# Kernel optimization log

Hardware: AMD Instinct MI355X
Metric: run time of the kernel (lower is better)

The kernel has to match this reference:

```python
import jax, jax.numpy as jnp
import numpy as np

N = 100000
E = 600000
G = 8
HID = 128
HEADS = 4
C = HID // HEADS  # 32


def setup_inputs() -> dict:
    key = jax.random.key(0)
    ks = jax.random.split(key, 32)
    s = 0.05
    node_numeric = jax.random.normal(ks[0], (N, 8), jnp.float32)
    node_cat0 = jax.random.randint(ks[1], (N,), 0, 32)
    node_cat1 = jax.random.randint(ks[2], (N,), 0, 64)
    edge_numeric = jax.random.normal(ks[3], (E, 4), jnp.float32)
    edge_cat0 = jax.random.randint(ks[4], (E,), 0, 16)
    edge_cat1 = jax.random.randint(ks[5], (E,), 0, 100)
    src = jax.random.randint(ks[6], (E,), 0, N)
    dst = jax.random.randint(ks[7], (E,), 0, N)
    dst = jnp.where(dst == src, (dst + 1) % N, dst)  # GATConv removes self-loops before adding its own
    edge_index = jnp.stack([src, dst])
    batch = jnp.sort(jax.random.randint(ks[8], (N,), 0, G))
    recipe = jax.random.normal(ks[9], (G, 16), jnp.float32)
    return dict(
        node_numeric=node_numeric, node_cat0=node_cat0, node_cat1=node_cat1,
        edge_numeric=edge_numeric, edge_cat0=edge_cat0, edge_cat1=edge_cat1,
        edge_index=edge_index, batch=batch, recipe=recipe,
        emb_node0=jax.random.normal(ks[10], (32, 6), jnp.float32) * s,
        emb_node1=jax.random.normal(ks[11], (64, 8), jnp.float32) * s,
        emb_edge0=jax.random.normal(ks[12], (16, 4), jnp.float32) * s,
        emb_edge1=jax.random.normal(ks[13], (100, 10), jnp.float32) * s,
        W_in=jax.random.normal(ks[14], (38, HID), jnp.float32) * s,
        b_in=jnp.zeros((HID,), jnp.float32),
        W_edge=jax.random.normal(ks[15], (18, HID), jnp.float32) * s,
        b_edge=jnp.zeros((HID,), jnp.float32),
        gat_lin=jax.random.normal(ks[16], (3, HID, HID), jnp.float32) * s,
        gat_lin_edge=jax.random.normal(ks[17], (3, HID, HID), jnp.float32) * s,
        att_src=jax.random.normal(ks[18], (3, HEADS, C), jnp.float32) * s,
        att_dst=jax.random.normal(ks[19], (3, HEADS, C), jnp.float32) * s,
        att_edge=jax.random.normal(ks[20], (3, HEADS, C), jnp.float32) * s,
        gat_bias=jnp.zeros((3, HID), jnp.float32),
        W_r1=jax.random.normal(ks[21], (HID, HID), jnp.float32) * s,
        b_r1=jnp.zeros((HID,), jnp.float32),
        W_r2=jax.random.normal(ks[22], (HID, 1), jnp.float32) * s,
        b_r2=jnp.zeros((1,), jnp.float32),
    )


def _segment_softmax(logits, seg, num):
    m = jax.ops.segment_max(logits, seg, num_segments=num)
    ex = jnp.exp(logits - m[seg])
    s = jax.ops.segment_sum(ex, seg, num_segments=num)
    return ex / s[seg]


def _forward(node_numeric, edge_numeric, recipe,
             emb_node0, emb_node1, emb_edge0, emb_edge1,
             W_in, b_in, W_edge, b_edge,
             gat_lin, gat_lin_edge, att_src, att_dst, att_edge, gat_bias,
             W_r1, b_r1, W_r2, b_r2,
             node_cat0, node_cat1, edge_cat0, edge_cat1, edge_index, batch):
    n = node_numeric.shape[0]
    src, dst = edge_index[0], edge_index[1]
    # node encoding: numeric + categorical embeddings + broadcast recipe
    h = jnp.concatenate([node_numeric, emb_node0[node_cat0], emb_node1[node_cat1], recipe[batch]], axis=1)
    h = jax.nn.relu(h @ W_in + b_in)
    # edge encoding (shared across GAT layers)
    e = jnp.concatenate([edge_numeric, emb_edge0[edge_cat0], emb_edge1[edge_cat1]], axis=1)
    e = e @ W_edge + b_edge
    # self-loops with fill_value='mean': per-dst mean of incoming edge_attr
    cnt = jax.ops.segment_sum(jnp.ones((e.shape[0],), e.dtype), dst, num_segments=n)
    loop = jax.ops.segment_sum(e, dst, num_segments=n) / jnp.maximum(cnt, 1.0)[:, None]
    ar = jnp.arange(n)
    src_a = jnp.concatenate([src, ar])
    dst_a = jnp.concatenate([dst, ar])
    e_a = jnp.concatenate([e, loop], axis=0)  # [E+N, HID]
    for l in range(gat_lin.shape[0]):
        x = (h @ gat_lin[l]).reshape(n, HEADS, C)          # shared lin_src/lin_dst
        ee = (e_a @ gat_lin_edge[l]).reshape(-1, HEADS, C)
        a_s = jnp.sum(x * att_src[l], axis=-1)   # [N, HEADS]
        a_d = jnp.sum(x * att_dst[l], axis=-1)
        a_e = jnp.sum(ee * att_edge[l], axis=-1)  # [E+N, HEADS]
        logits = jax.nn.leaky_relu(a_s[src_a] + a_d[dst_a] + a_e, negative_slope=0.2)
        alpha = _segment_softmax(logits, dst_a, n)  # segment softmax over dst
        out = jax.ops.segment_sum(x[src_a] * alpha[:, :, None], dst_a, num_segments=n)
        h = jax.nn.relu(out.reshape(n, HID) + gat_bias[l])  # dropout off (eval)
    g = jax.ops.segment_sum(h, batch, num_segments=G)  # global_add_pool
    g = jax.nn.relu(g @ W_r1 + b_r1)
    return g @ W_r2 + b_r2  # [G, 1]


def reference(node_numeric, node_cat0, node_cat1, edge_numeric, edge_cat0, edge_cat1,
              edge_index, batch, recipe,
              emb_node0, emb_node1, emb_edge0, emb_edge1,
              W_in, b_in, W_edge, b_edge,
              gat_lin, gat_lin_edge, att_src, att_dst, att_edge, gat_bias,
              W_r1, b_r1, W_r2, b_r2):
    return _forward(node_numeric, edge_numeric, recipe,
                    emb_node0, emb_node1, emb_edge0, emb_edge1,
                    W_in, b_in, W_edge, b_edge,
                    gat_lin, gat_lin_edge, att_src, att_dst, att_edge, gat_bias,
                    W_r1, b_r1, W_r2, b_r2,
                    node_cat0, node_cat1, edge_cat0, edge_cat1, edge_index, batch)
```

## Files before the change

kernel.cpp:

```cpp
#include <hip/hip_runtime.h>
#include <math.h>

#define HID 128

typedef float f32x4 __attribute__((ext_vector_type(4)));
typedef short bf16x8 __attribute__((ext_vector_type(8)));
typedef unsigned int uint32;

__device__ __forceinline__ float leaky02(float z) { return z >= 0.f ? z : 0.2f * z; }
__device__ __forceinline__ unsigned short f2bf(float f) {
  uint32 u = __float_as_uint(f);
  u = (u + 0x7fff + ((u >> 16) & 1)) >> 16;
  return (unsigned short)u;
}
__device__ __forceinline__ float bf2f(uint32 us) { return __uint_as_float(us << 16); }
__device__ __forceinline__ float bflo(uint32 w) { return __uint_as_float(w << 16); }
__device__ __forceinline__ float bfhi(uint32 w) { return __uint_as_float(w & 0xffff0000u); }

__global__ void k_enc(const float* __restrict__ nodenum, const int* __restrict__ c0,
                      const int* __restrict__ c1, const int* __restrict__ batch,
                      const float* __restrict__ recipe,
                      const float* __restrict__ e0, const float* __restrict__ e1,
                      const float* __restrict__ Win, const float* __restrict__ bin,
                      unsigned short* __restrict__ hb, int n) {
  __shared__ float f[8][40];
  __shared__ int idx[8][3];
  int t = threadIdx.x;
  int col = t & 127;
  int half = t >> 7;
  float w[40];
#pragma unroll
  for (int k = 0; k < 38; k++) w[k] = Win[k * 128 + col];
  w[38] = 0.f;
  w[39] = 0.f;
  float bias = bin[col];
  int ntiles = (n + 7) / 8;
  for (int tile = blockIdx.x; tile < ntiles; tile += gridDim.x) {
    int base = tile * 8;
    if (t < 64) {
      int r = t >> 3, k = t & 7;
      int v = base + r;
      f[r][k] = (v < n) ? nodenum[(size_t)v * 8 + k] : 0.f;
    } else if (t < 88) {
      int j = t - 64;
      int r = j / 3, which = j - r * 3;
      int v = base + r;
      int val = 0;
      if (v < n) val = (which == 0) ? c0[v] : ((which == 1) ? c1[v] : batch[v]);
      idx[r][which] = val;
    } else if (t >= 240) {
      int r = t - 240;
      if (r < 8) { f[r][38] = 0.f; f[r][39] = 0.f; }
    }
    __syncthreads();
    if (t < 240) {
      int r = t / 30, k = t - r * 30;
      float val;
      if (k < 6) val = e0[idx[r][0] * 6 + k];
      else if (k < 14) val = e1[idx[r][1] * 8 + (k - 6)];
      else val = recipe[idx[r][2] * 16 + (k - 14)];
      f[r][8 + k] = val;
    }
    __syncthreads();
#pragma unroll
    for (int rr = 0; rr < 4; rr++) {
      int r = half * 4 + rr;
      int v = base + r;
      float acc = bias;
#pragma unroll
      for (int k4 = 0; k4 < 10; k4++) {
        float4 fv = *(const float4*)(&f[r][k4 * 4]);
        acc += fv.x * w[k4 * 4] + fv.y * w[k4 * 4 + 1] + fv.z * w[k4 * 4 + 2] +
               fv.w * w[k4 * 4 + 3];
      }
      if (v < n) hb[(size_t)v * 128 + col] = f2bf(fmaxf(acc, 0.f));
    }
    __syncthreads();
  }
}

__global__ void k_prep(const float* __restrict__ gle, const float* __restrict__ atte,
                       const float* __restrict__ We, const float* __restrict__ be,
                       float* __restrict__ P, float* __restrict__ q) {
  __shared__ float M[128 * 4];
  int t = threadIdx.x;
  for (int l = 0; l < 3; l++) {
    {
      int k = t;
#pragma unroll
      for (int hh = 0; hh < 4; hh++) {
        float acc = 0.f;
        for (int c = 0; c < 32; c++)
          acc += gle[l * 16384 + k * 128 + hh * 32 + c] * atte[l * 128 + hh * 32 + c];
        M[k * 4 + hh] = acc;
      }
    }
    __syncthreads();
    if (t < 72) {
      int j = t >> 2, hh = t & 3;
      float acc = 0.f;
      for (int k = 0; k < 128; k++) acc += We[j * 128 + k] * M[k * 4 + hh];
      P[(l * 18 + j) * 4 + hh] = acc;
    }
    if (t < 4) {
      float acc = 0.f;
      for (int k = 0; k < 128; k++) acc += be[k] * M[k * 4 + t];
      q[l * 4 + t] = acc;
    }
    __syncthreads();
  }
}

__global__ void k_wprep(const float* __restrict__ glin, unsigned short* __restrict__ WbfT) {
  int idx = blockIdx.x * 256 + threadIdx.x;
  if (idx >= 3 * 128 * 128) return;
  int l = idx >> 14;
  int rem = idx & 16383;
  int col = rem >> 7;
  int k = rem & 127;
  WbfT[idx] = f2bf(glin[(l << 14) + k * 128 + col]);
}

__global__ void k_deg(const int* __restrict__ dst, int* __restrict__ cnt, int E) {
  int i = blockIdx.x * 256 + threadIdx.x;
  if (i < E) atomicAdd(&cnt[dst[i]], 1);
}

__global__ void k_ae(const float* __restrict__ enum_, const int* __restrict__ ec0,
                     const int* __restrict__ ec1, const int* __restrict__ dst,
                     const int* __restrict__ srcarr,
                     const float* __restrict__ ee0, const float* __restrict__ ee1,
                     const float* __restrict__ P, const float* __restrict__ q,
                     int* __restrict__ cursor, float* __restrict__ ae3,
                     int* __restrict__ srcc, int E) {
  __shared__ float Ps[216];
  __shared__ float qs[12];
  int t = threadIdx.x;
  for (int i = t; i < 216; i += 256) Ps[i] = P[i];
  if (t < 12) qs[t] = q[t];
  __syncthreads();
  int i = blockIdx.x * 256 + t;
  if (i >= E) return;
  float raw[18];
  float4 nm = *(const float4*)(enum_ + (size_t)i * 4);
  raw[0] = nm.x; raw[1] = nm.y; raw[2] = nm.z; raw[3] = nm.w;
  int a0 = ec0[i], a1 = ec1[i];
  float4 eb0 = *(const float4*)(ee0 + a0 * 4);
  raw[4] = eb0.x; raw[5] = eb0.y; raw[6] = eb0.z; raw[7] = eb0.w;
#pragma unroll
  for (int j = 0; j < 10; j++) raw[8 + j] = ee1[a1 * 10 + j];
  int d = dst[i];
  int pos = atomicAdd(&cursor[d], 1);
  srcc[pos] = srcarr[i];
#pragma unroll
  for (int l = 0; l < 3; l++) {
    float o[4];
#pragma unroll
    for (int hh = 0; hh < 4; hh++) {
      float acc = qs[l * 4 + hh];
#pragma unroll
      for (int j = 0; j < 18; j++) acc += raw[j] * Ps[(l * 18 + j) * 4 + hh];
      o[hh] = acc;
    }
    *(float4*)(ae3 + ((size_t)l * E + pos) * 4) = make_float4(o[0], o[1], o[2], o[3]);
  }
}

__global__ void k_loopmean(const float* __restrict__ ae3, const int* __restrict__ rowptr,
                           float* __restrict__ aeL, int n, int E) {
  int v = blockIdx.x * 256 + threadIdx.x;
  if (v >= n) return;
  int beg = rowptr[v], end = rowptr[v + 1];
  float inv = (end > beg) ? 1.f / (float)(end - beg) : 0.f;
#pragma unroll
  for (int l = 0; l < 3; l++) {
    float4 s = make_float4(0.f, 0.f, 0.f, 0.f);
    const float4* base = (const float4*)(ae3 + (size_t)l * E * 4);
    for (int j = beg; j < end; j++) {
      float4 a = base[j];
      s.x += a.x; s.y += a.y; s.z += a.z; s.w += a.w;
    }
    *(float4*)(aeL + ((size_t)l * n + v) * 4) =
        make_float4(s.x * inv, s.y * inv, s.z * inv, s.w * inv);
  }
}

__global__ void k_scan1(const int* __restrict__ cnt, int* __restrict__ excl,
                        int* __restrict__ bsum, int n) {
  __shared__ int sh[256];
  int t = threadIdx.x;
  int i = blockIdx.x * 256 + t;
  int v = (i < n) ? cnt[i] : 0;
  sh[t] = v;
  __syncthreads();
  for (int off = 1; off < 256; off <<= 1) {
    int add = (t >= off) ? sh[t - off] : 0;
    __syncthreads();
    sh[t] += add;
    __syncthreads();
  }
  if (i < n) excl[i] = sh[t] - v;
  if (t == 255) bsum[blockIdx.x] = sh[255];
}

__global__ void k_scan2(int* __restrict__ bsum, int nb) {
  __shared__ int sh[512];
  int t = threadIdx.x;
  int v = (t < nb) ? bsum[t] : 0;
  sh[t] = v;
  __syncthreads();
  for (int off = 1; off < 512; off <<= 1) {
    int add = (t >= off) ? sh[t - off] : 0;
    __syncthreads();
    sh[t] += add;
    __syncthreads();
  }
  if (t < nb) bsum[t] = sh[t] - v;
}

__global__ void k_scan3(int* __restrict__ rowptr, const int* __restrict__ boff,
                        int* __restrict__ cursor, int n, int E) {
  int i = blockIdx.x * 256 + threadIdx.x;
  if (i < n) {
    int val = rowptr[i] + boff[i >> 8];
    rowptr[i] = val;
    cursor[i] = val;
  }
  if (i == 0) rowptr[n] = E;
}

__global__ void __launch_bounds__(512, 4)
k_x(const unsigned short* __restrict__ hb, const unsigned short* __restrict__ WbfT,
    const float* __restrict__ att_s, const float* __restrict__ att_d,
    unsigned short* __restrict__ xb, float* __restrict__ a_s,
    float* __restrict__ a_d, int n) {
  __shared__ unsigned short hs[64 * 128];
  int t = threadIdx.x;
  int w = t >> 6, l = t & 63;
  int ch = w >> 2, wr = w & 3;
  int lr = l & 15, lg = l >> 4;
  bf16x8 bfrag[4][4];
#pragma unroll
  for (int ct = 0; ct < 4; ct++) {
#pragma unroll
    for (int ks = 0; ks < 4; ks++) {
      int col = ch * 64 + ct * 16 + lr;
      int k0 = ks * 32 + lg * 8;
      bfrag[ct][ks] = *(const bf16x8*)(WbfT + col * 128 + k0);
    }
  }
  float avs[4], avd[4];
#pragma unroll
  for (int ct = 0; ct < 4; ct++) {
    avs[ct] = att_s[ch * 64 + ct * 16 + lr];
    avd[ct] = att_d[ch * 64 + ct * 16 + lr];
  }
  for (int tb = blockIdx.x * 64; tb < n; tb += gridDim.x * 64) {
    __syncthreads();
#pragma unroll
    for (int i = 0; i < 2; i++) {
      int idx = t + i * 512;
      int r = idx >> 4, c = idx & 15;
      uint4 vv = make_uint4(0, 0, 0, 0);
      if (tb + r < n) vv = *(const uint4*)(hb + (size_t)(tb + r) * 128 + c * 8);
      *(uint4*)(&hs[r * 128 + ((c ^ (r & 7)) * 8)]) = vv;
    }
    __syncthreads();
    f32x4 acc[4];
#pragma unroll
    for (int ct = 0; ct < 4; ct++) acc[ct] = (f32x4){0.f, 0.f, 0.f, 0.f};
#pragma unroll
    for (int ks = 0; ks < 4; ks++) {
      int r = wr * 16 + lr;
      int c = ks * 4 + lg;
      bf16x8 a = *(const bf16x8*)(&hs[r * 128 + ((c ^ (r & 7)) * 8)]);
#pragma unroll
      for (int ct = 0; ct < 4; ct++)
        acc[ct] = __builtin_amdgcn_mfma_f32_16x16x32_bf16(a, bfrag[ct][ks], acc[ct], 0, 0, 0);
    }
#pragma unroll
    for (int j = 0; j < 4; j++) {
      int row = tb + wr * 16 + lg * 4 + j;
      bool ok = row < n;
      if (ok) {
#pragma unroll
        for (int ct = 0; ct < 4; ct++)
          xb[(size_t)row * 128 + ch * 64 + ct * 16 + lr] = f2bf(acc[ct][j]);
      }
      float psA = acc[0][j] * avs[0] + acc[1][j] * avs[1];
      float pdA = acc[0][j] * avd[0] + acc[1][j] * avd[1];
      float psB = acc[2][j] * avs[2] + acc[3][j] * avs[3];
      float pdB = acc[2][j] * avd[2] + acc[3][j] * avd[3];
#pragma unroll
      for (int m = 1; m <= 8; m <<= 1) {
        psA += __shfl_xor(psA, m); pdA += __shfl_xor(pdA, m);
        psB += __shfl_xor(psB, m); pdB += __shfl_xor(pdB, m);
      }
      if (lr == 0 && ok) {
        a_s[(size_t)row * 4 + ch * 2] = psA;
        a_s[(size_t)row * 4 + ch * 2 + 1] = psB;
        a_d[(size_t)row * 4 + ch * 2] = pdA;
        a_d[(size_t)row * 4 + ch * 2 + 1] = pdB;
      }
    }
  }
}

__global__ void k_agg(const unsigned short* __restrict__ xb, const float* __restrict__ a_s,
                      const float* __restrict__ a_d, const float* __restrict__ ae3,
                      const float* __restrict__ aeL,
                      const int* __restrict__ rowptr, const int* __restrict__ srcc,
                      const float* __restrict__ bias,
                      unsigned short* __restrict__ hbout, int n, int E, int l) {
  int wid = threadIdx.x >> 6;
  int v = blockIdx.x * 4 + wid;
  if (v >= n) return;
  int lane = threadIdx.x & 63;
  int el = lane >> 2;
  int hh = lane & 3;
  float ad_own = a_d[(size_t)v * 4 + hh];
  float as_own = a_s[(size_t)v * 4 + hh];
  float aeL_own = aeL[((size_t)l * n + v) * 4 + hh];
  float m_own = leaky02(as_own + ad_own + aeL_own);
  float s_own = 1.f;
  int c2 = lane * 2;
  int headO = lane >> 4;
  const char* xB = (const char*)xb;
  uint32 coff = (uint32)c2 * 2u;
  uint32 wv = *(const uint32*)(xB + ((uint32)v << 8) + coff);
  float a0 = bflo(wv);
  float a1 = bfhi(wv);
  int beg = rowptr[v], end = rowptr[v + 1];
  const float* aeB = ae3 + (size_t)l * E * 4;
  for (int cb = beg; cb < end; cb += 16) {
    int ne = end - cb;
    if (ne > 16) ne = 16;
    float logit = -1e30f;
    int srcE = 0;
    if (el < ne) {
      int j = cb + el;
      srcE = srcc[j];
      float asrc = a_s[(size_t)srcE * 4 + hh];
      float aev = aeB[(size_t)j * 4 + hh];
      logit = leaky02(asrc + ad_own + aev);
    }
    float cm = logit;
    cm = fmaxf(cm, __shfl_xor(cm, 4));
    cm = fmaxf(cm, __shfl_xor(cm, 8));
    cm = fmaxf(cm, __shfl_xor(cm, 16));
    cm = fmaxf(cm, __shfl_xor(cm, 32));
    float mn_own = fmaxf(m_own, cm);
    float p = (el < ne) ? __expf(logit - mn_own) : 0.f;
    float ps = p;
    ps += __shfl_xor(ps, 4);
    ps += __shfl_xor(ps, 8);
    ps += __shfl_xor(ps, 16);
    ps += __shfl_xor(ps, 32);
    float c_own = __expf(m_own - mn_own);
    m_own = mn_own;
    s_own = s_own * c_own + ps;
    float cO = __shfl(c_own, headO);
    a0 *= cO;
    a1 *= cO;
    int e = 0;
    for (; e + 2 <= ne; e += 2) {
      int se0 = __builtin_amdgcn_readlane(srcE, e * 4);
      int se1 = __builtin_amdgcn_readlane(srcE, e * 4 + 4);
      float p0 = __shfl(p, e * 4 + headO);
      float p1 = __shfl(p, e * 4 + 4 + headO);
      uint32 x0 = *(const uint32*)(xB + ((uint32)se0 << 8) + coff);
      uint32 x1 = *(const uint32*)(xB + ((uint32)se1 << 8) + coff);
      a0 += p0 * bflo(x0) + p1 * bflo(x1);
      a1 += p0 * bfhi(x0) + p1 * bfhi(x1);
    }
    if (e < ne) {
      int se = __builtin_amdgcn_readlane(srcE, e * 4);
      float pC = __shfl(p, e * 4 + headO);
      uint32 xw = *(const uint32*)(xB + ((uint32)se << 8) + coff);
      a0 += pC * bflo(xw);
      a1 += pC * bfhi(xw);
    }
  }
  float sO = __shfl(s_own, headO);
  float r0 = fmaxf(a0 / sO + bias[l * HID + c2], 0.f);
  float r1 = fmaxf(a1 / sO + bias[l * HID + c2 + 1], 0.f);
  uint32 pk = (uint32)f2bf(r0) | ((uint32)f2bf(r1) << 16);
  *(uint32*)(hbout + (size_t)v * HID + c2) = pk;
}

__global__ void k_pool(const unsigned short* __restrict__ hb, const int* __restrict__ batch,
                       float* __restrict__ g, int n) {
  int t = threadIdx.x;
  int per = (n + gridDim.x - 1) / gridDim.x;
  int start = blockIdx.x * per;
  int end = min(n, start + per);
  float acc = 0.f;
  int cur = -1;
  for (int v = start; v < end; v++) {
    int b = batch[v];
    if (b != cur) {
      if (cur >= 0) atomicAdd(&g[cur * 128 + t], acc);
      acc = 0.f;
      cur = b;
    }
    acc += bf2f((uint32)hb[(size_t)v * 128 + t]);
  }
  if (cur >= 0) atomicAdd(&g[cur * 128 + t], acc);
}

__global__ void k_head(const float* __restrict__ g, const float* __restrict__ Wr1,
                       const float* __restrict__ br1, const float* __restrict__ Wr2,
                       const float* __restrict__ br2, float* __restrict__ out, int G_) {
  __shared__ float gl[8 * 128];
  __shared__ float red[128];
  int t = threadIdx.x;
  for (int i = t; i < G_ * 128; i += 128) gl[i] = g[i];
  __syncthreads();
  for (int i = 0; i < G_; i++) {
    float acc = br1[t];
    for (int k = 0; k < 128; k++) acc += gl[i * 128 + k] * Wr1[k * 128 + t];
    float hv = fmaxf(acc, 0.f);
    red[t] = hv * Wr2[t];
    __syncthreads();
    if (t == 0) {
      float s = br2[0];
      for (int k = 0; k < 128; k++) s += red[k];
      out[i] = s;
    }
    __syncthreads();
  }
}

extern "C" void kernel_launch(void* const* d_in, const int* in_sizes, int n_in,
                              void* d_out, int out_size, void* d_ws, size_t ws_size,
                              hipStream_t stream) {
  const float* node_numeric = (const float*)d_in[0];
  const int* node_cat0 = (const int*)d_in[1];
  const int* node_cat1 = (const int*)d_in[2];
  const float* edge_numeric = (const float*)d_in[3];
  const int* edge_cat0 = (const int*)d_in[4];
  const int* edge_cat1 = (const int*)d_in[5];
  const int* edge_index = (const int*)d_in[6];
  const int* batch = (const int*)d_in[7];
  const float* recipe = (const float*)d_in[8];
  const float* emb_node0 = (const float*)d_in[9];
  const float* emb_node1 = (const float*)d_in[10];
  const float* emb_edge0 = (const float*)d_in[11];
  const float* emb_edge1 = (const float*)d_in[12];
  const float* W_in = (const float*)d_in[13];
  const float* b_in = (const float*)d_in[14];
  const float* W_edge = (const float*)d_in[15];
  const float* b_edge = (const float*)d_in[16];
  const float* gat_lin = (const float*)d_in[17];
  const float* gat_lin_edge = (const float*)d_in[18];
  const float* att_src = (const float*)d_in[19];
  const float* att_dst = (const float*)d_in[20];
  const float* att_edge = (const float*)d_in[21];
  const float* gat_bias = (const float*)d_in[22];
  const float* W_r1 = (const float*)d_in[23];
  const float* b_r1 = (const float*)d_in[24];
  const float* W_r2 = (const float*)d_in[25];
  const float* b_r2 = (const float*)d_in[26];

  int N = in_sizes[0] / 8;
  int E = in_sizes[3] / 4;
  int Gn = in_sizes[8] / 16;
  const int* srcArr = edge_index;
  const int* dstArr = edge_index + E;

  char* ws = (char*)d_ws;
  size_t o = 0;
  auto alloc = [&](size_t b) {
    char* p = ws + o;
    o = (o + b + 255) & ~(size_t)255;
    return p;
  };
  unsigned short* hbf = (unsigned short*)alloc((size_t)N * 128 * 2);
  unsigned short* xbf = (unsigned short*)alloc((size_t)N * 128 * 2);
  float* ae3 = (float*)alloc((size_t)E * 12 * 4);
  float* aeL = (float*)alloc((size_t)N * 12 * 4);
  float* a_s = (float*)alloc((size_t)N * 4 * 4);
  float* a_d = (float*)alloc((size_t)N * 4 * 4);
  float* P = (float*)alloc(216 * 4);
  float* q = (float*)alloc(12 * 4);
  unsigned short* WbfT = (unsigned short*)alloc(3 * 128 * 128 * 2);
  int* cnt = (int*)alloc((size_t)N * 4);
  int* rowptr = (int*)alloc((size_t)(N + 1) * 4);
  int* cursor = (int*)alloc((size_t)N * 4);
  int* bsum = (int*)alloc(512 * 4);
  int* srcc = (int*)alloc((size_t)E * 4);
  float* g = (float*)alloc((size_t)Gn * 128 * 4);
  (void)ws_size;

  (void)hipMemsetAsync(cnt, 0, (size_t)N * 4, stream);
  (void)hipMemsetAsync(g, 0, (size_t)Gn * 128 * 4, stream);

  int nbl = (N + 255) / 256;
  int ebl = (E + 255) / 256;

  k_enc<<<2048, 256, 0, stream>>>(node_numeric, node_cat0, node_cat1, batch, recipe,
                                  emb_node0, emb_node1, W_in, b_in, hbf, N);
  k_prep<<<1, 128, 0, stream>>>(gat_lin_edge, att_edge, W_edge, b_edge, P, q);
  k_wprep<<<192, 256, 0, stream>>>(gat_lin, WbfT);
  k_deg<<<ebl, 256, 0, stream>>>(dstArr, cnt, E);
  k_scan1<<<nbl, 256, 0, stream>>>(cnt, rowptr, bsum, N);
  k_scan2<<<1, 512, 0, stream>>>(bsum, nbl);
  k_scan3<<<nbl, 256, 0, stream>>>(rowptr, bsum, cursor, N, E);
  k_ae<<<ebl, 256, 0, stream>>>(edge_numeric, edge_cat0, edge_cat1, dstArr, srcArr,
                                emb_edge0, emb_edge1, P, q, cursor, ae3, srcc, E);
  k_loopmean<<<nbl, 256, 0, stream>>>(ae3, rowptr, aeL, N, E);

  for (int l = 0; l < 3; l++) {
    k_x<<<512, 512, 0, stream>>>(hbf, WbfT + l * 16384, att_src + l * 128,
                                 att_dst + l * 128, xbf, a_s, a_d, N);
    k_agg<<<(N + 3) / 4, 256, 0, stream>>>(xbf, a_s, a_d, ae3, aeL, rowptr, srcc,
                                           gat_bias, hbf, N, E, l);
  }
  k_pool<<<1024, 128, 0, stream>>>(hbf, batch, g, N);
  k_head<<<1, 128, 0, stream>>>(g, W_r1, b_r1, W_r2, b_r2, (float*)d_out, Gn);
}
```

Baseline: 442.0 us.

## Remap agg lanes to head-owned columns, parallelize prep and head kernels

The aggregation kernel now gives each lane columns inside its own head (col0 = head*32 + slot*2). This lets it use its own softmax rescale and sum without cross-lane shuffles, and it fetches edge weights with ds_swizzle in a fully unrolled 16-edge block. The change also splits k_prep across 3 blocks (one per layer) and k_head across G blocks with a tree reduction, removing serial single-block loops. The cost is a strided column access pattern per wave, which may make the gathered row loads less contiguous across lanes.

```diff
diff --git a/kernel.cpp b/kernel.cpp
--- a/kernel.cpp
+++ b/kernel.cpp
@@ -82,32 +82,29 @@
 __global__ void k_prep(const float* __restrict__ gle, const float* __restrict__ atte,
                        const float* __restrict__ We, const float* __restrict__ be,
                        float* __restrict__ P, float* __restrict__ q) {
-  __shared__ float M[128 * 4];
-  int t = threadIdx.x;
-  for (int l = 0; l < 3; l++) {
-    {
-      int k = t;
-#pragma unroll
-      for (int hh = 0; hh < 4; hh++) {
-        float acc = 0.f;
-        for (int c = 0; c < 32; c++)
-          acc += gle[l * 16384 + k * 128 + hh * 32 + c] * atte[l * 128 + hh * 32 + c];
-        M[k * 4 + hh] = acc;
-      }
-    }
-    __syncthreads();
-    if (t < 72) {
-      int j = t >> 2, hh = t & 3;
-      float acc = 0.f;
-      for (int k = 0; k < 128; k++) acc += We[j * 128 + k] * M[k * 4 + hh];
-      P[(l * 18 + j) * 4 + hh] = acc;
-    }
-    if (t < 4) {
-      float acc = 0.f;
-      for (int k = 0; k < 128; k++) acc += be[k] * M[k * 4 + t];
-      q[l * 4 + t] = acc;
-    }
-    __syncthreads();
+  __shared__ float M[512];
+  int l = blockIdx.x;
+  int t = threadIdx.x;
+#pragma unroll
+  for (int i = 0; i < 2; i++) {
+    int idx = t + i * 256;
+    int k = idx >> 2, hh = idx & 3;
+    float acc = 0.f;
+    for (int c = 0; c < 32; c++)
+      acc += gle[l * 16384 + k * 128 + hh * 32 + c] * atte[l * 128 + hh * 32 + c];
+    M[k * 4 + hh] = acc;
+  }
+  __syncthreads();
+  if (t < 72) {
+    int j = t >> 2, hh = t & 3;
+    float acc = 0.f;
+    for (int k = 0; k < 128; k++) acc += We[j * 128 + k] * M[k * 4 + hh];
+    P[(l * 18 + j) * 4 + hh] = acc;
+  } else if (t < 76) {
+    int hh = t - 72;
+    float acc = 0.f;
+    for (int k = 0; k < 128; k++) acc += be[k] * M[k * 4 + hh];
+    q[l * 4 + hh] = acc;
   }
 }
 
@@ -306,6 +303,16 @@
   }
 }
 
+#define AGG_EDGE(ec, srcu)                                                              \
+  if ((ec) < ne) {                                                                      \
+    float pe = __uint_as_float((uint32)__builtin_amdgcn_ds_swizzle(                     \
+        (int)(srcu), (((((ec) & 7)) * 4) << 5) | 3));                                   \
+    int se = __builtin_amdgcn_readlane(srcE, (ec) * 4);                                 \
+    uint32 xw = *(const uint32*)(xB + ((uint32)se << 8) + coff);                        \
+    a0 += pe * bflo(xw);                                                                \
+    a1 += pe * bfhi(xw);                                                                \
+  }
+
 __global__ void k_agg(const unsigned short* __restrict__ xb, const float* __restrict__ a_s,
                       const float* __restrict__ a_d, const float* __restrict__ ae3,
                       const float* __restrict__ aeL,
@@ -316,17 +323,16 @@
   int v = blockIdx.x * 4 + wid;
   if (v >= n) return;
   int lane = threadIdx.x & 63;
-  int el = lane >> 2;
+  int sl = lane >> 2;
   int hh = lane & 3;
   float ad_own = a_d[(size_t)v * 4 + hh];
   float as_own = a_s[(size_t)v * 4 + hh];
   float aeL_own = aeL[((size_t)l * n + v) * 4 + hh];
   float m_own = leaky02(as_own + ad_own + aeL_own);
   float s_own = 1.f;
-  int c2 = lane * 2;
-  int headO = lane >> 4;
+  int col0 = hh * 32 + sl * 2;
   const char* xB = (const char*)xb;
-  uint32 coff = (uint32)c2 * 2u;
+  uint32 coff = (uint32)col0 * 2u;
   uint32 wv = *(const uint32*)(xB + ((uint32)v << 8) + coff);
   float a0 = bflo(wv);
   float a1 = bfhi(wv);
@@ -337,8 +343,8 @@
     if (ne > 16) ne = 16;
     float logit = -1e30f;
     int srcE = 0;
-    if (el < ne) {
-      int j = cb + el;
+    if (sl < ne) {
+      int j = cb + sl;
       srcE = srcc[j];
       float asrc = a_s[(size_t)srcE * 4 + hh];
       float aev = aeB[(size_t)j * 4 + hh];
@@ -350,7 +356,7 @@
     cm = fmaxf(cm, __shfl_xor(cm, 16));
     cm = fmaxf(cm, __shfl_xor(cm, 32));
     float mn_own = fmaxf(m_own, cm);
-    float p = (el < ne) ? __expf(logit - mn_own) : 0.f;
+    float p = (sl < ne) ? __expf(logit - mn_own) : 0.f;
     float ps = p;
     ps += __shfl_xor(ps, 4);
     ps += __shfl_xor(ps, 8);
@@ -359,33 +365,34 @@
     float c_own = __expf(m_own - mn_own);
     m_own = mn_own;
     s_own = s_own * c_own + ps;
-    float cO = __shfl(c_own, headO);
-    a0 *= cO;
-    a1 *= cO;
-    int e = 0;
-    for (; e + 2 <= ne; e += 2) {
-      int se0 = __builtin_amdgcn_readlane(srcE, e * 4);
-      int se1 = __builtin_amdgcn_readlane(srcE, e * 4 + 4);
-      float p0 = __shfl(p, e * 4 + headO);
-      float p1 = __shfl(p, e * 4 + 4 + headO);
-      uint32 x0 = *(const uint32*)(xB + ((uint32)se0 << 8) + coff);
-      uint32 x1 = *(const uint32*)(xB + ((uint32)se1 << 8) + coff);
-      a0 += p0 * bflo(x0) + p1 * bflo(x1);
-      a1 += p0 * bfhi(x0) + p1 * bfhi(x1);
-    }
-    if (e < ne) {
-      int se = __builtin_amdgcn_readlane(srcE, e * 4);
-      float pC = __shfl(p, e * 4 + headO);
-      uint32 xw = *(const uint32*)(xB + ((uint32)se << 8) + coff);
-      a0 += pC * bflo(xw);
-      a1 += pC * bfhi(xw);
-    }
-  }
-  float sO = __shfl(s_own, headO);
-  float r0 = fmaxf(a0 / sO + bias[l * HID + c2], 0.f);
-  float r1 = fmaxf(a1 / sO + bias[l * HID + c2 + 1], 0.f);
+    a0 *= c_own;
+    a1 *= c_own;
+    float pswap = __shfl(p, lane ^ 32);
+    float plo = (lane < 32) ? p : pswap;
+    float phi = (lane < 32) ? pswap : p;
+    uint32 plo_u = __float_as_uint(plo);
+    uint32 phi_u = __float_as_uint(phi);
+    AGG_EDGE(0, plo_u)
+    AGG_EDGE(1, plo_u)
+    AGG_EDGE(2, plo_u)
+    AGG_EDGE(3, plo_u)
+    AGG_EDGE(4, plo_u)
+    AGG_EDGE(5, plo_u)
+    AGG_EDGE(6, plo_u)
+    AGG_EDGE(7, plo_u)
+    AGG_EDGE(8, phi_u)
+    AGG_EDGE(9, phi_u)
+    AGG_EDGE(10, phi_u)
+    AGG_EDGE(11, phi_u)
+    AGG_EDGE(12, phi_u)
+    AGG_EDGE(13, phi_u)
+    AGG_EDGE(14, phi_u)
+    AGG_EDGE(15, phi_u)
+  }
+  float r0 = fmaxf(a0 / s_own + bias[l * HID + col0], 0.f);
+  float r1 = fmaxf(a1 / s_own + bias[l * HID + col0 + 1], 0.f);
   uint32 pk = (uint32)f2bf(r0) | ((uint32)f2bf(r1) << 16);
-  *(uint32*)(hbout + (size_t)v * HID + c2) = pk;
+  *(uint32*)(hbout + (size_t)v * HID + col0) = pk;
 }
 
 __global__ void k_pool(const unsigned short* __restrict__ hb, const int* __restrict__ batch,
@@ -411,24 +418,22 @@
 __global__ void k_head(const float* __restrict__ g, const float* __restrict__ Wr1,
                        const float* __restrict__ br1, const float* __restrict__ Wr2,
                        const float* __restrict__ br2, float* __restrict__ out, int G_) {
-  __shared__ float gl[8 * 128];
+  __shared__ float gl[128];
   __shared__ float red[128];
-  int t = threadIdx.x;
-  for (int i = t; i < G_ * 128; i += 128) gl[i] = g[i];
+  int i = blockIdx.x;
+  int t = threadIdx.x;
+  gl[t] = g[i * 128 + t];
   __syncthreads();
-  for (int i = 0; i < G_; i++) {
-    float acc = br1[t];
-    for (int k = 0; k < 128; k++) acc += gl[i * 128 + k] * Wr1[k * 128 + t];
-    float hv = fmaxf(acc, 0.f);
-    red[t] = hv * Wr2[t];
-    __syncthreads();
-    if (t == 0) {
-      float s = br2[0];
-      for (int k = 0; k < 128; k++) s += red[k];
-      out[i] = s;
-    }
-    __syncthreads();
-  }
+  float acc = br1[t];
+  for (int k = 0; k < 128; k++) acc += gl[k] * Wr1[k * 128 + t];
+  float hv = fmaxf(acc, 0.f);
+  red[t] = hv * Wr2[t];
+  __syncthreads();
+  for (int off = 64; off >= 1; off >>= 1) {
+    if (t < off) red[t] += red[t + off];
+    __syncthreads();
+  }
+  if (t == 0) out[i] = red[0] + br2[0];
 }
 
 extern "C" void kernel_launch(void* const* d_in, const int* in_sizes, int n_in,
@@ -500,7 +505,7 @@
 
   k_enc<<<2048, 256, 0, stream>>>(node_numeric, node_cat0, node_cat1, batch, recipe,
                                   emb_node0, emb_node1, W_in, b_in, hbf, N);
-  k_prep<<<1, 128, 0, stream>>>(gat_lin_edge, att_edge, W_edge, b_edge, P, q);
+  k_prep<<<3, 256, 0, stream>>>(gat_lin_edge, att_edge, W_edge, b_edge, P, q);
   k_wprep<<<192, 256, 0, stream>>>(gat_lin, WbfT);
   k_deg<<<ebl, 256, 0, stream>>>(dstArr, cnt, E);
   k_scan1<<<nbl, 256, 0, stream>>>(cnt, rowptr, bsum, N);
@@ -517,5 +522,5 @@
                                            gat_bias, hbf, N, E, l);
   }
   k_pool<<<1024, 128, 0, stream>>>(hbf, batch, g, N);
-  k_head<<<1, 128, 0, stream>>>(g, W_r1, b_r1, W_r2, b_r2, (float*)d_out, Gn);
-}
+  k_head<<<Gn, 128, 0, stream>>>(g, W_r1, b_r1, W_r2, b_r2, (float*)d_out, Gn);
+}
```

Result: slower. 462.2 us (+4.6%).
